# Kernel optimization log

Measured on AMD Instinct MI355X. Metric: run time of the kernel, lower is better.

## Reference

```python
import jax, jax.numpy as jnp
import numpy as np

FACTOR = 2
DIM = 3
F3 = FACTOR ** DIM  # 8 children per voxel
N = 1_000_000
C = 64
K = 4  # exactly K active children per voxel -> static output size M = N*K


def setup_inputs() -> dict:
    key = jax.random.key(0)
    k1, k2, k3 = jax.random.split(key, 3)
    coords = jax.random.randint(k1, (N, DIM + 1), 0, 512, dtype=jnp.int32)
    feats = jax.random.normal(k2, (N, C), dtype=jnp.float32)
    # binary subdivision mask with exactly K ones per row (static nonzero count)
    r = jax.random.uniform(k3, (N, F3))
    rank = jnp.argsort(jnp.argsort(r, axis=-1), axis=-1)
    sub = (rank < K).astype(jnp.int32)
    return {"feats": feats, "coords": coords, "sub": sub}


def reference(feats, coords, sub):
    n = coords.shape[0]
    M = n * K  # static total number of output voxels
    # flat nonzero indices over [N*F3]; sorted, equivalent to torch's
    # row-major nonzero() + repeat_interleave index construction
    flat = jnp.nonzero(sub.reshape(-1), size=M, fill_value=0)[0]
    idx = flat // F3      # parent voxel index (== repeat_interleave(arange(N), N_leaf))
    subidx = flat % F3    # child slot within the 2x2x2 cell
    # new_coords: scale spatial coords by factor, add per-child octant offset
    scale = jnp.array([1] + [FACTOR] * DIM, dtype=coords.dtype)
    off = jnp.stack(
        [jnp.zeros_like(subidx)] + [(subidx // FACTOR**i) % FACTOR for i in range(DIM)],
        axis=1,
    ).astype(coords.dtype)
    new_coords = (coords * scale)[idx] + off  # [M, 1+DIM]
    # channel -> spatial: reshape feats to [N*F3, C/F3], gather child features
    x_feats = feats.reshape(n * F3, C // F3)
    new_feats = x_feats[idx * F3 + subidx]  # == x_feats[flat], [M, C/F3]
    return new_feats, new_coords
```

## Files before the change

kernel.cpp:

```cpp
#include <hip/hip_runtime.h>
#include <hip/hip_bf16.h>


typedef float f4 __attribute__((ext_vector_type(4)));
typedef int   i4 __attribute__((ext_vector_type(4)));

#define VPB 64
#define ROWP 68

__global__ __launch_bounds__(256) void sc2s_kernel(
    const float* __restrict__ feats,
    const int*   __restrict__ coords,
    const int*   __restrict__ sub,
    float*       __restrict__ out_feats,
    float*       __restrict__ out_coords,
    int N) {
  __shared__ __align__(16) float sf[VPB * ROWP];
  __shared__ int sj[VPB];
  __shared__ __align__(16) int sc[VPB * 4];

  int b   = blockIdx.x;
  int tid = threadIdx.x;
  int v0  = b * VPB;

  {
    int vi = tid >> 2, w0 = (tid & 3) << 4;
    const f4* src = reinterpret_cast<const f4*>(feats + (size_t)(v0 + vi) * 64 + w0);
    f4* dst = reinterpret_cast<f4*>(&sf[vi * ROWP + w0]);
    #pragma unroll
    for (int q = 0; q < 4; ++q) dst[q] = src[q];
  }
  if (tid < VPB) {
    const i4* s4 = reinterpret_cast<const i4*>(sub) + (size_t)(v0 + tid) * 2;
    i4 a = s4[0], bb = s4[1];
    unsigned m = (unsigned)(a.x != 0)
               | ((unsigned)(a.y != 0) << 1)
               | ((unsigned)(a.z != 0) << 2)
               | ((unsigned)(a.w != 0) << 3)
               | ((unsigned)(bb.x != 0) << 4)
               | ((unsigned)(bb.y != 0) << 5)
               | ((unsigned)(bb.z != 0) << 6)
               | ((unsigned)(bb.w != 0) << 7);
    int j0 = __ffs(m) - 1; m &= m - 1;
    int j1 = __ffs(m) - 1; m &= m - 1;
    int j2 = __ffs(m) - 1; m &= m - 1;
    int j3 = __ffs(m) - 1;
    sj[tid] = j0 | (j1 << 8) | (j2 << 16) | (j3 << 24);
  } else if (tid < 2 * VPB) {
    int vi = tid - VPB;
    reinterpret_cast<i4*>(sc)[vi] = reinterpret_cast<const i4*>(coords)[v0 + vi];
  }
  __syncthreads();

  f4* ofb = reinterpret_cast<f4*>(out_feats) + (size_t)b * (VPB * 8);
  #pragma unroll
  for (int p = 0; p < 2; ++p) {
    int cc   = tid + p * 256;
    int vi   = cc >> 3;
    int k    = (cc >> 1) & 3;
    int half = cc & 1;
    int j    = (sj[vi] >> (k * 8)) & 0xff;
    f4 v = *reinterpret_cast<const f4*>(&sf[vi * ROWP + j * 8 + half * 4]);
    __builtin_nontemporal_store(v, ofb + cc);
  }
  {
    int cc = tid;
    int vi = cc >> 2;
    int k  = cc & 3;
    int j  = (sj[vi] >> (k * 8)) & 0xff;
    const int* c = &sc[vi * 4];
    f4 o;
    o.x = (float)c[0];
    o.y = (float)(c[1] * 2 + (j & 1));
    o.z = (float)(c[2] * 2 + ((j >> 1) & 1));
    o.w = (float)(c[3] * 2 + ((j >> 2) & 1));
    __builtin_nontemporal_store(o, reinterpret_cast<f4*>(out_coords) + (size_t)b * (VPB * 4) + cc);
  }
}

extern "C" void kernel_launch(void* const* d_in, const int* in_sizes, int n_in,
                              void* d_out, int out_size, void* d_ws, size_t ws_size,
                              hipStream_t stream) {
  const float* feats  = (const float*)d_in[0];
  const int*   coords = (const int*)d_in[1];
  const int*   sub    = (const int*)d_in[2];

  int M = out_size / 12;
  int N = M / 4;
  float* out_feats  = (float*)d_out;
  float* out_coords = (float*)d_out + (size_t)M * 8;

  int grid = (N + VPB - 1) / VPB;
  sc2s_kernel<<<grid, 256, 0, stream>>>(feats, coords, sub, out_feats, out_coords, N);
}
```

Baseline: 80.84 us.

## Load only feature lines containing active children instead of full rows

Instead of staging every voxel's full 64-float feature row in shared memory, the kernel builds a compact list of 32-byte child-pair lines that hold at least one active child. It uses a wave prefix scan over per-voxel line counts, then gathers only those lines from global memory and scatters active children into a packed shared buffer. This is meant to cut global read traffic for features, since inactive child pairs are never loaded. In exchange it adds a scan, an extra barrier, a dummy slot that absorbs inactive writes, and 32-byte granular loads that may not reduce actual DRAM sector traffic much.

```diff
diff --git a/kernel.cpp b/kernel.cpp
--- a/kernel.cpp
+++ b/kernel.cpp
@@ -6,7 +6,6 @@
 typedef int   i4 __attribute__((ext_vector_type(4)));
 
 #define VPB 64
-#define ROWP 68
 
 __global__ __launch_bounds__(256) void sc2s_kernel(
     const float* __restrict__ feats,
@@ -15,21 +14,16 @@
     float*       __restrict__ out_feats,
     float*       __restrict__ out_coords,
     int N) {
-  __shared__ __align__(16) float sf[VPB * ROWP];
-  __shared__ int sj[VPB];
+  __shared__ int sm[VPB];
+  __shared__ int slines[VPB * 4];
+  __shared__ int s_total;
+  __shared__ __align__(16) float schunk[(VPB * 8 + 1) * 4];
   __shared__ __align__(16) int sc[VPB * 4];
 
   int b   = blockIdx.x;
   int tid = threadIdx.x;
   int v0  = b * VPB;
 
-  {
-    int vi = tid >> 2, w0 = (tid & 3) << 4;
-    const f4* src = reinterpret_cast<const f4*>(feats + (size_t)(v0 + vi) * 64 + w0);
-    f4* dst = reinterpret_cast<f4*>(&sf[vi * ROWP + w0]);
-    #pragma unroll
-    for (int q = 0; q < 4; ++q) dst[q] = src[q];
-  }
   if (tid < VPB) {
     const i4* s4 = reinterpret_cast<const i4*>(sub) + (size_t)(v0 + tid) * 2;
     i4 a = s4[0], bb = s4[1];
@@ -41,33 +35,66 @@
                | ((unsigned)(bb.y != 0) << 5)
                | ((unsigned)(bb.z != 0) << 6)
                | ((unsigned)(bb.w != 0) << 7);
-    int j0 = __ffs(m) - 1; m &= m - 1;
-    int j1 = __ffs(m) - 1; m &= m - 1;
-    int j2 = __ffs(m) - 1; m &= m - 1;
-    int j3 = __ffs(m) - 1;
-    sj[tid] = j0 | (j1 << 8) | (j2 << 16) | (j3 << 24);
+    sm[tid] = (int)m;
+    unsigned lm = (m | (m >> 1)) & 0x55u;
+    int lcount = __popc(lm);
+    int x = lcount;
+    #pragma unroll
+    for (int d = 1; d < 64; d <<= 1) {
+      int v = __shfl_up(x, d);
+      if (tid >= d) x += v;
+    }
+    int base = x - lcount;
+    if (tid == VPB - 1) s_total = x;
+    int o = base;
+    #pragma unroll
+    for (int l = 0; l < 4; ++l) {
+      if ((m >> (2 * l)) & 3u) slines[o++] = (tid << 2) | l;
+    }
   } else if (tid < 2 * VPB) {
     int vi = tid - VPB;
     reinterpret_cast<i4*>(sc)[vi] = reinterpret_cast<const i4*>(coords)[v0 + vi];
   }
   __syncthreads();
 
+  int L4 = s_total * 4;
+  #pragma unroll
+  for (int p = 0; p < 4; ++p) {
+    int idx = tid + p * 256;
+    if (p < 2 || idx < L4) {
+      int e     = slines[idx >> 2];
+      int vi    = e >> 2;
+      int l     = e & 3;
+      int q     = idx & 3;
+      int child = l * 2 + (q >> 1);
+      int half  = q & 1;
+      f4 v = reinterpret_cast<const f4*>(feats)[(size_t)(v0 + vi) * 16 + child * 2 + half];
+      unsigned m = (unsigned)sm[vi];
+      int active = (m >> child) & 1;
+      int rank   = __popc(m & ((1u << child) - 1u));
+      int cc     = active ? (vi * 8 + rank * 2 + half) : (VPB * 8);
+      reinterpret_cast<f4*>(schunk)[cc] = v;
+    }
+  }
+  __syncthreads();
+
   f4* ofb = reinterpret_cast<f4*>(out_feats) + (size_t)b * (VPB * 8);
   #pragma unroll
   for (int p = 0; p < 2; ++p) {
-    int cc   = tid + p * 256;
-    int vi   = cc >> 3;
-    int k    = (cc >> 1) & 3;
-    int half = cc & 1;
-    int j    = (sj[vi] >> (k * 8)) & 0xff;
-    f4 v = *reinterpret_cast<const f4*>(&sf[vi * ROWP + j * 8 + half * 4]);
+    int cc = tid + p * 256;
+    f4 v = reinterpret_cast<const f4*>(schunk)[cc];
     __builtin_nontemporal_store(v, ofb + cc);
   }
   {
     int cc = tid;
     int vi = cc >> 2;
     int k  = cc & 3;
-    int j  = (sj[vi] >> (k * 8)) & 0xff;
+    unsigned m = (unsigned)sm[vi];
+    #pragma unroll
+    for (int q = 0; q < 3; ++q) {
+      if (q < k) m &= (m - 1u);
+    }
+    int j = __ffs(m) - 1;
     const int* c = &sc[vi * 4];
     f4 o;
     o.x = (float)c[0];
```

Measured after the change: 82.26 us. Within noise of the previous version (+1.7%).
